# Kernel tuning notes

Measured on AMD Instinct MI355X. Metric: run time of the kernel, lower is better.

The kernel has to match this reference:

```python
import jax, jax.numpy as jnp
import numpy as np

S = 2048        # tokens (single prefill sequence)
HID = 3584      # hidden_size
H = 16          # num query heads
KV = 8          # num kv heads
D = 256         # head_dim
WINDOW = 1024   # sliding window size
CAP = 50.0      # logit softcap
SCALE = 256.0 ** -0.5   # query_pre_attn_scalar ** -0.5
THETA = 10000.0


def setup_inputs() -> dict:
    key = jax.random.key(0)
    ks = jax.random.split(key, 5)
    hidden_states = jax.random.normal(ks[0], (S, HID), dtype=jnp.float32)
    positions = jnp.arange(S, dtype=jnp.int32)
    Wq = jax.random.normal(ks[1], (HID, H * D), dtype=jnp.float32) * 0.02
    Wk = jax.random.normal(ks[2], (HID, KV * D), dtype=jnp.float32) * 0.02
    Wv = jax.random.normal(ks[3], (HID, KV * D), dtype=jnp.float32) * 0.02
    Wo = jax.random.normal(ks[4], (H * D, HID), dtype=jnp.float32) * 0.02
    return {"hidden_states": hidden_states, "positions": positions,
            "Wq": Wq, "Wk": Wk, "Wv": Wv, "Wo": Wo}


def _rope_neox(x, positions):
    # x: [S, n_heads, D]; neox-style: rotate halves, full rotary_dim == D
    half = D // 2
    inv_freq = 1.0 / (THETA ** (jnp.arange(0, half, dtype=jnp.float32) * 2.0 / D))
    freqs = positions.astype(jnp.float32)[:, None] * inv_freq[None, :]  # [S, half]
    cos = jnp.cos(freqs)[:, None, :].astype(x.dtype)
    sin = jnp.sin(freqs)[:, None, :].astype(x.dtype)
    x1, x2 = x[..., :half], x[..., half:]
    return jnp.concatenate([x1 * cos - x2 * sin, x2 * cos + x1 * sin], axis=-1)


def reference(hidden_states, positions, Wq, Wk, Wv, Wo):
    # QKV projections (no bias)
    q = (hidden_states @ Wq).reshape(S, H, D)
    k = (hidden_states @ Wk).reshape(S, KV, D)
    v = (hidden_states @ Wv).reshape(S, KV, D)
    q = _rope_neox(q, positions)
    k = _rope_neox(k, positions)
    # grouped-query attention: G query heads per kv head
    G = H // KV
    qg = q.reshape(S, KV, G, D)
    scores = jnp.einsum('qkgd,skd->kgqs', qg, k) * jnp.asarray(SCALE, q.dtype)
    # logit soft-capping
    scores = CAP * jnp.tanh(scores / CAP)
    # causal + sliding-window mask
    i = positions[:, None]
    j = positions[None, :]
    mask = (j <= i) & ((i - j) < WINDOW)   # [S, S]
    neg = jnp.finfo(scores.dtype).min
    scores = jnp.where(mask[None, None, :, :], scores, neg)
    p = jax.nn.softmax(scores, axis=-1)
    attn = jnp.einsum('kgqs,skd->qkgd', p, v).reshape(S, H * D)
    return attn @ Wo
```

## Files before the change

### kernel.cpp

```cpp
#include <hip/hip_runtime.h>
#include <stdint.h>

#define S 2048
#define HID 3584
#define NH 16
#define NKV 8
#define DH 256
#define WINDOW 1024
#define SCALE 0.0625f
#define CAP 50.0f

typedef short s16x8 __attribute__((ext_vector_type(8)));
typedef float f32x4 __attribute__((ext_vector_type(4)));

__device__ __forceinline__ short f2bf(float f) {
  union { float f; uint32_t u; } c; c.f = f;
  uint32_t u = c.u;
  uint32_t r = (u + 0x7FFFu + ((u >> 16) & 1u)) >> 16;
  return (short)r;
}
__device__ __forceinline__ float bf2f(short s) {
  union { uint32_t u; float f; } c;
  c.u = ((uint32_t)(uint16_t)s) << 16;
  return c.f;
}
__device__ __forceinline__ void gll16(const void* g, void* l) {
  __builtin_amdgcn_global_load_lds((const __attribute__((address_space(1))) void*)g,
                                   (__attribute__((address_space(3))) void*)l, 16, 0, 0);
}

__global__ void rope_table_kernel(float2* __restrict__ tbl) {
  int idx = blockIdx.x * 256 + threadIdx.x;
  int s = idx >> 7, i = idx & 127;
  float inv = __expf(-(float)i * (9.210340371976184f / 128.0f));
  float fr = (float)s * inv;
  tbl[idx] = make_float2(cosf(fr), sinf(fr));
}

__global__ void conv_hs_kernel(const float* __restrict__ src, short* __restrict__ dst) {
  int gid = blockIdx.x * 256 + threadIdx.x;
  float4 a = *(const float4*)&src[(size_t)gid * 8];
  float4 b = *(const float4*)&src[(size_t)gid * 8 + 4];
  s16x8 o;
  o[0] = f2bf(a.x); o[1] = f2bf(a.y); o[2] = f2bf(a.z); o[3] = f2bf(a.w);
  o[4] = f2bf(b.x); o[5] = f2bf(b.y); o[6] = f2bf(b.z); o[7] = f2bf(b.w);
  *(s16x8*)&dst[(size_t)gid * 8] = o;
}

__global__ __launch_bounds__(256)
void transpose_all_kernel(const float* __restrict__ Wq, const float* __restrict__ Wk,
                          const float* __restrict__ Wv, const float* __restrict__ Wo,
                          short* __restrict__ Wt, short* __restrict__ WtO)
{
  __shared__ __align__(16) short t[64][76];
  int b = blockIdx.x;
  const float* src; short* dst; int K, N, lb;
  if (b < 3584)      { src = Wq; dst = Wt;                       K = HID;  N = 4096; lb = b; }
  else if (b < 5376) { src = Wk; dst = Wt + (size_t)4096 * HID;  K = HID;  N = 2048; lb = b - 3584; }
  else if (b < 7168) { src = Wv; dst = Wt + (size_t)6144 * HID;  K = HID;  N = 2048; lb = b - 5376; }
  else               { src = Wo; dst = WtO;                      K = 4096; N = HID;  lb = b - 7168; }
  int ntn = N >> 6;
  int tn = lb % ntn, tk = lb / ntn;
  int tid = threadIdx.x;
  int c = tid & 63, rg = tid >> 6;
  #pragma unroll
  for (int i = 0; i < 4; ++i) {
    int r0 = i * 16 + rg * 4;
    short tmp[4];
    #pragma unroll
    for (int j = 0; j < 4; ++j)
      tmp[j] = f2bf(src[(size_t)(tk * 64 + r0 + j) * N + tn * 64 + c]);
    *(short4*)&t[c][r0] = *(short4*)tmp;
  }
  __syncthreads();
  #pragma unroll
  for (int it = 0; it < 2; ++it) {
    int flat = it * 256 + tid;
    int n = flat >> 3, kc = flat & 7;
    *(s16x8*)&dst[(size_t)(tn * 64 + n) * K + tk * 64 + kc * 8] = *(s16x8*)&t[n][kc * 8];
  }
}

__global__ __launch_bounds__(256)
void transpose_v_kernel(const short* __restrict__ vsb, short* __restrict__ vtb)
{
  __shared__ short t[64][74];
  int b = blockIdx.x;
  int kv = b >> 7;
  int rem = b & 127;
  int s0 = (rem >> 2) * 64, d0 = (rem & 3) * 64;
  const short* src = vsb + ((size_t)kv * S + s0) * DH + d0;
  short* dst = vtb + ((size_t)kv * DH + d0) * S + s0;
  int tid = threadIdx.x;
  int c = tid & 63, sb = (tid >> 6) * 16;
  #pragma unroll
  for (int ss = 0; ss < 16; ++ss)
    t[c][sb + ss] = src[(size_t)(sb + ss) * DH + c];
  __syncthreads();
  #pragma unroll
  for (int it = 0; it < 2; ++it) {
    int flat = it * 256 + tid;
    int r = flat >> 3, cc = (flat & 7) * 8;
    *(s16x8*)&dst[(size_t)r * S + cc] = *(s16x8*)&t[r][cc];
  }
}

__global__ __launch_bounds__(256, 2)
void qkv_gemm_kernel(const short* __restrict__ hsb, const short* __restrict__ Wt,
                     short* __restrict__ qb, short* __restrict__ kbuf,
                     short* __restrict__ vsb)
{
  __shared__ __align__(16) short Asb[256 * 64];
  __shared__ __align__(16) short Bsb[128 * 64];
  int bid = blockIdx.x;
  int i = bid >> 3;
  int bm = i & 7;
  int bn = (bid & 7) * 8 + (i >> 3);
  int m0 = bm * 256, n0 = bn * 128;
  int tid = threadIdx.x, w = tid >> 6, lane = tid & 63;
  int lr = lane & 15, lk = lane >> 4;
  int wm = (w >> 1) * 128, wn = (w & 1) * 64;
  int r7 = lr & 7;
  int abase = (wm + lr) * 64 + ((lk ^ r7) * 8);
  int bbase = (wn + lr) * 64 + ((lk ^ r7) * 8);
  int row8 = tid >> 3;
  int colsw = ((tid & 7) ^ (row8 & 7)) * 8;
  const short* srcA = hsb + (size_t)(m0 + row8) * HID + colsw;
  const short* srcB = Wt + (size_t)(n0 + row8) * HID + colsw;
  f32x4 acc[8][4] = {};
  for (int t = 0; t < HID / 64; ++t) {
    const short* sa = srcA + t * 64;
    const short* sb = srcB + t * 64;
    #pragma unroll
    for (int r = 0; r < 8; ++r)
      gll16(sa + (size_t)(r * 32) * HID, Asb + r * 2048 + w * 512);
    #pragma unroll
    for (int r = 0; r < 4; ++r)
      gll16(sb + (size_t)(r * 32) * HID, Bsb + r * 2048 + w * 512);
    __syncthreads();
    s16x8 bf[4][2];
    #pragma unroll
    for (int nf = 0; nf < 4; ++nf)
      #pragma unroll
      for (int kh = 0; kh < 2; ++kh)
        bf[nf][kh] = *(const s16x8*)&Bsb[(bbase + nf * 16 * 64) ^ (kh * 32)];
    #pragma unroll
    for (int mh = 0; mh < 2; ++mh) {
      s16x8 af[4][2];
      #pragma unroll
      for (int mf = 0; mf < 4; ++mf)
        #pragma unroll
        for (int kh = 0; kh < 2; ++kh)
          af[mf][kh] = *(const s16x8*)&Asb[(abase + (mh * 64 + mf * 16) * 64) ^ (kh * 32)];
      __builtin_amdgcn_s_setprio(1);
      #pragma unroll
      for (int mf = 0; mf < 4; ++mf)
        #pragma unroll
        for (int nf = 0; nf < 4; ++nf) {
          acc[mh * 4 + mf][nf] = __builtin_amdgcn_mfma_f32_16x16x32_bf16(
              af[mf][0], bf[nf][0], acc[mh * 4 + mf][nf], 0, 0, 0);
          acc[mh * 4 + mf][nf] = __builtin_amdgcn_mfma_f32_16x16x32_bf16(
              af[mf][1], bf[nf][1], acc[mh * 4 + mf][nf], 0, 0, 0);
        }
      __builtin_amdgcn_s_setprio(0);
    }
    __syncthreads();
  }
  int region = (n0 < 4096) ? 0 : ((n0 < 6144) ? 1 : 2);
  #pragma unroll
  for (int m = 0; m < 8; ++m) {
    int srow_b = m0 + wm + m * 16 + lk * 4;
    #pragma unroll
    for (int n = 0; n < 4; ++n) {
      int ncol = n0 + wn + n * 16 + lr;
      #pragma unroll
      for (int r = 0; r < 4; ++r) {
        int srow = srow_b + r;
        short bv = f2bf(acc[m][n][r]);
        if (region == 0) {
          int h = ncol >> 8, d = ncol & 255;
          qb[((size_t)h * S + srow) * DH + d] = bv;
        } else if (region == 1) {
          int c = ncol - 4096; int kv = c >> 8, d = c & 255;
          kbuf[((size_t)kv * S + srow) * DH + d] = bv;
        } else {
          int c = ncol - 6144; int kv = c >> 8, d = c & 255;
          vsb[((size_t)kv * S + srow) * DH + d] = bv;
        }
      }
    }
  }
}

__global__ __launch_bounds__(256)
void out_gemm_kernel(const short* __restrict__ attnb, const short* __restrict__ WtO,
                     float* __restrict__ out)
{
  __shared__ __align__(16) short Asb[128 * 64];
  __shared__ __align__(16) short Bsb[128 * 64];
  int bid = blockIdx.x;
  int flat = (bid & 7) * 56 + (bid >> 3);
  int bn = flat >> 4, bm = flat & 15;
  int m0 = bm * 128, n0 = bn * 128;
  int tid = threadIdx.x, w = tid >> 6, lane = tid & 63;
  int lr = lane & 15, lk = lane >> 4;
  int wm = (w >> 1) * 64, wn = (w & 1) * 64;
  int r7 = lr & 7;
  int abase = (wm + lr) * 64 + ((lk ^ r7) * 8);
  int bbase = (wn + lr) * 64 + ((lk ^ r7) * 8);
  int row8 = tid >> 3;
  int colsw = ((tid & 7) ^ (row8 & 7)) * 8;
  const short* srcA = attnb + (size_t)(m0 + row8) * 4096 + colsw;
  const short* srcB = WtO + (size_t)(n0 + row8) * 4096 + colsw;
  f32x4 acc[4][4] = {};
  for (int t = 0; t < 4096 / 64; ++t) {
    const short* sa = srcA + t * 64;
    const short* sb = srcB + t * 64;
    #pragma unroll
    for (int r = 0; r < 4; ++r)
      gll16(sa + (size_t)(r * 32) * 4096, Asb + r * 2048 + w * 512);
    #pragma unroll
    for (int r = 0; r < 4; ++r)
      gll16(sb + (size_t)(r * 32) * 4096, Bsb + r * 2048 + w * 512);
    __syncthreads();
    s16x8 af[4][2], bf[4][2];
    #pragma unroll
    for (int f = 0; f < 4; ++f)
      #pragma unroll
      for (int kh = 0; kh < 2; ++kh) {
        af[f][kh] = *(const s16x8*)&Asb[(abase + f * 16 * 64) ^ (kh * 32)];
        bf[f][kh] = *(const s16x8*)&Bsb[(bbase + f * 16 * 64) ^ (kh * 32)];
      }
    __builtin_amdgcn_s_setprio(1);
    #pragma unroll
    for (int mf = 0; mf < 4; ++mf)
      #pragma unroll
      for (int nf = 0; nf < 4; ++nf) {
        acc[mf][nf] = __builtin_amdgcn_mfma_f32_16x16x32_bf16(
            af[mf][0], bf[nf][0], acc[mf][nf], 0, 0, 0);
        acc[mf][nf] = __builtin_amdgcn_mfma_f32_16x16x32_bf16(
            af[mf][1], bf[nf][1], acc[mf][nf], 0, 0, 0);
      }
    __builtin_amdgcn_s_setprio(0);
    __syncthreads();
  }
  #pragma unroll
  for (int mf = 0; mf < 4; ++mf) {
    int srow_b = m0 + wm + mf * 16 + lk * 4;
    #pragma unroll
    for (int nf = 0; nf < 4; ++nf) {
      int ncol = n0 + wn + nf * 16 + lr;
      #pragma unroll
      for (int r = 0; r < 4; ++r)
        out[(size_t)(srow_b + r) * HID + ncol] = acc[mf][nf][r];
    }
  }
}

__global__ void rope_kernel(short* __restrict__ qb, short* __restrict__ kbuf,
                            const float2* __restrict__ tbl)
{
  int gid = blockIdx.x * 256 + threadIdx.x;
  int row = gid >> 4, ch = gid & 15;
  short* base = (row < NH * S) ? (qb + (size_t)row * DH)
                               : (kbuf + (size_t)(row - NH * S) * DH);
  int s = row & (S - 1);
  int i0 = ch * 8;
  s16x8 x1 = *(s16x8*)(base + i0);
  s16x8 x2 = *(s16x8*)(base + 128 + i0);
  s16x8 y1, y2;
  #pragma unroll
  for (int j = 0; j < 8; ++j) {
    float2 cs = tbl[s * 128 + i0 + j];
    float a = bf2f(x1[j]), b = bf2f(x2[j]);
    y1[j] = f2bf(a * cs.x - b * cs.y);
    y2[j] = f2bf(b * cs.x + a * cs.y);
  }
  *(s16x8*)(base + i0) = y1;
  *(s16x8*)(base + 128 + i0) = y2;
}

__global__ __launch_bounds__(512)
void attn_kernel(const short* __restrict__ qb, const short* __restrict__ kbuf,
                 const short* __restrict__ vtb, short* __restrict__ attnb)
{
  __shared__ __align__(16) short Klds[2][64][256];
  __shared__ __align__(16) short Vlds[2][256][64];
  __shared__ __align__(16) short Plds[8][16][72];
  int bid = blockIdx.x;
  int qt = 31 - (bid >> 4), h = bid & 15;
  int kv = h >> 1;
  int q0 = qt * 64;
  int tid = threadIdx.x;
  int w = tid >> 6, lane = tid & 63;
  int g = w >> 2, wsub = w & 3;
  int gtid = tid & 255;
  int lr = lane & 15, lk = lane >> 4;
  int qrow_base = q0 + wsub * 16;
  s16x8 qf[8];
  const short* qrow = qb + ((size_t)h * S + (qrow_base + lr)) * DH;
  #pragma unroll
  for (int kb = 0; kb < 8; ++kb)
    qf[kb] = *(const s16x8*)(qrow + kb * 32 + lk * 8);
  f32x4 acc_o[16] = {};
  float l_r[4] = {0.0f, 0.0f, 0.0f, 0.0f};
  int tlo = (q0 >= WINDOW - 1) ? ((q0 - (WINDOW - 1)) >> 6) : 0;
  int thi = q0 >> 6;
  const short* kbase = kbuf + (size_t)kv * S * DH;
  const short* vbase = vtb + (size_t)kv * DH * S;

  s16x8 kpf[8], vpf[8];
  auto loadRegs = [&](int t) {
    int k0 = t * 64;
    #pragma unroll
    for (int it = 0; it < 8; ++it) {
      int flat = it * 256 + gtid;
      int r = flat >> 5, cg = flat & 31;
      kpf[it] = *(const s16x8*)(kbase + (size_t)(k0 + r) * DH + cg * 8);
    }
    #pragma unroll
    for (int it = 0; it < 8; ++it) {
      int flat = it * 256 + gtid;
      int r = flat >> 3, cg = flat & 7;
      vpf[it] = *(const s16x8*)(vbase + (size_t)r * S + k0 + cg * 8);
    }
  };
  auto writeLds = [&]() {
    #pragma unroll
    for (int it = 0; it < 8; ++it) {
      int flat = it * 256 + gtid;
      int r = flat >> 5, cg = flat & 31;
      *(s16x8*)&Klds[g][r][(cg ^ (r & 7)) * 8] = kpf[it];
    }
    #pragma unroll
    for (int it = 0; it < 8; ++it) {
      int flat = it * 256 + gtid;
      int r = flat >> 3, cg = flat & 7;
      *(s16x8*)&Vlds[g][r][(cg ^ (r & 7)) * 8] = vpf[it];
    }
  };

  int tg0 = tlo + g;
  int n_all = thi - tlo + 1;
  int jmax = (n_all + 1) >> 1;
  if (tg0 <= thi) loadRegs(tg0);
  for (int j = 0; j < jmax; ++j) {
    int t = tg0 + 2 * j;
    bool active = (t <= thi);
    if (active) writeLds();
    __syncthreads();
    if (active && t + 2 <= thi) loadRegs(t + 2);
    if (active) {
      int k0 = t * 64;
      f32x4 sc4[4] = {};
      __builtin_amdgcn_s_setprio(1);
      #pragma unroll
      for (int kb = 0; kb < 8; ++kb)
        #pragma unroll
        for (int ni = 0; ni < 4; ++ni) {
          int row = ni * 16 + lr;
          s16x8 b = *(const s16x8*)&Klds[g][row][(((kb << 2) | lk) ^ (row & 7)) * 8];
          sc4[ni] = __builtin_amdgcn_mfma_f32_16x16x32_bf16(qf[kb], b, sc4[ni], 0, 0, 0);
        }
      __builtin_amdgcn_s_setprio(0);
      bool interior = (k0 + 63 <= qrow_base) && (qrow_base + 15 - k0 < WINDOW);
      #pragma unroll
      for (int ni = 0; ni < 4; ++ni)
        #pragma unroll
        for (int r = 0; r < 4; ++r) {
          float raw = sc4[ni][r];
          float e = __expf(-fabsf(raw) * (2.0f * SCALE / CAP));
          float wgt = raw > 0.0f ? e : 1.0f;
          float p = __expf(-2.0f * CAP * __fdividef(wgt, 1.0f + e));
          if (!interior) {
            int qg = qrow_base + lk * 4 + r;
            int kg = k0 + ni * 16 + lr;
            bool valid = (kg <= qg) && (qg - kg < WINDOW);
            p = valid ? p : 0.0f;
          }
          sc4[ni][r] = p;
          l_r[r] += p;
        }
      #pragma unroll
      for (int ni = 0; ni < 4; ++ni)
        #pragma unroll
        for (int r = 0; r < 4; ++r)
          Plds[w][lk * 4 + r][ni * 16 + lr] = f2bf(sc4[ni][r]);
      s16x8 pa0 = *(const s16x8*)&Plds[w][lr][lk * 8];
      s16x8 pa1 = *(const s16x8*)&Plds[w][lr][32 + lk * 8];
      __builtin_amdgcn_s_setprio(1);
      #pragma unroll
      for (int df = 0; df < 16; ++df) {
        int row = df * 16 + lr;
        s16x8 b0 = *(const s16x8*)&Vlds[g][row][((lk ^ (row & 7)) * 8)];
        s16x8 b1 = *(const s16x8*)&Vlds[g][row][(((4 + lk) ^ (row & 7)) * 8)];
        acc_o[df] = __builtin_amdgcn_mfma_f32_16x16x32_bf16(pa0, b0, acc_o[df], 0, 0, 0);
        acc_o[df] = __builtin_amdgcn_mfma_f32_16x16x32_bf16(pa1, b1, acc_o[df], 0, 0, 0);
      }
      __builtin_amdgcn_s_setprio(0);
    }
    __syncthreads();
  }
  float lsum[4];
  #pragma unroll
  for (int r = 0; r < 4; ++r) {
    float v = l_r[r];
    #pragma unroll
    for (int off = 1; off < 16; off <<= 1)
      v += __shfl_xor(v, off, 64);
    lsum[r] = v;
  }
  float* comb = (float*)&Klds[0][0][0];
  float* lcomb = (float*)&Vlds[0][0][0];
  if (g == 1) {
    #pragma unroll
    for (int df = 0; df < 16; ++df)
      #pragma unroll
      for (int r = 0; r < 4; ++r)
        comb[(size_t)(wsub * 16 + lk * 4 + r) * 256 + df * 16 + lr] = acc_o[df][r];
    if (lr == 0)
      #pragma unroll
      for (int r = 0; r < 4; ++r)
        lcomb[wsub * 16 + lk * 4 + r] = lsum[r];
  }
  __syncthreads();
  if (g == 0) {
    #pragma unroll
    for (int r = 0; r < 4; ++r) {
      int rowi = wsub * 16 + lk * 4 + r;
      float lt = lsum[r] + lcomb[rowi];
      float inv = 1.0f / lt;
      int srow = q0 + rowi;
      #pragma unroll
      for (int df = 0; df < 16; ++df) {
        float o = acc_o[df][r] + comb[(size_t)rowi * 256 + df * 16 + lr];
        attnb[(size_t)srow * (NH * DH) + h * DH + df * 16 + lr] = f2bf(o * inv);
      }
    }
  }
}

extern "C" void kernel_launch(void* const* d_in, const int* in_sizes, int n_in,
                              void* d_out, int out_size, void* d_ws, size_t ws_size,
                              hipStream_t stream) {
  const float* hs = (const float*)d_in[0];
  const float* Wq = (const float*)d_in[2];
  const float* Wk = (const float*)d_in[3];
  const float* Wv = (const float*)d_in[4];
  const float* Wo = (const float*)d_in[5];
  float* out = (float*)d_out;
  char* ws = (char*)d_ws;
  size_t off = 0;
  float2* tbl  = (float2*)(ws + off); off += 2097152;
  short* qb    = (short*)(ws + off);  off += 16777216;
  short* kbuf  = (short*)(ws + off);  off += 8388608;
  short* vtb   = (short*)(ws + off);  off += 8388608;
  short* attnb = (short*)(ws + off);  off += 16777216;
  short* hsb   = (short*)(ws + off);  off += 14680064;
  short* Wt    = (short*)(ws + off);  off += 58720256;
  short* WtO   = (short*)(ws + off);  off += 29360128;
  short* vsb   = (short*)(ws + off);  off += 8388608;

  hipLaunchKernelGGL(rope_table_kernel, dim3(1024), dim3(256), 0, stream, tbl);
  hipLaunchKernelGGL(conv_hs_kernel, dim3(3584), dim3(256), 0, stream, hs, hsb);
  hipLaunchKernelGGL(transpose_all_kernel, dim3(10752), dim3(256), 0, stream,
                     Wq, Wk, Wv, Wo, Wt, WtO);
  hipLaunchKernelGGL(qkv_gemm_kernel, dim3(512), dim3(256), 0, stream,
                     hsb, Wt, qb, kbuf, vsb);
  hipLaunchKernelGGL(transpose_v_kernel, dim3(1024), dim3(256), 0, stream,
                     vsb, vtb);
  hipLaunchKernelGGL(rope_kernel, dim3(3072), dim3(256), 0, stream, qb, kbuf, tbl);
  hipLaunchKernelGGL(attn_kernel, dim3(512), dim3(512), 0, stream,
                     qb, kbuf, vtb, attnb);
  hipLaunchKernelGGL(out_gemm_kernel, dim3(448), dim3(256), 0, stream,
                     attnb, WtO, out);
}
```

Before: 361.2 us.

## Split attention KV range across two blocks and combine partials in separate kernel

The attention kernel used to split each head's key tiles between two 256-thread groups inside one 512-thread block and merge them through LDS. It now launches twice as many 256-thread blocks, each covering alternate key tiles. Each block writes unnormalized fp32 partial outputs and row sums to workspace reused from the now-dead hidden-state and weight buffers. A new combine kernel adds the two partials, normalizes, and writes bf16. The aim is smaller blocks and less LDS per block for better occupancy and scheduling, at the cost of a large fp32 round trip through global memory and one extra launch.

```diff
diff --git a/kernel.cpp b/kernel.cpp
--- a/kernel.cpp
+++ b/kernel.cpp
@@ -280,23 +280,24 @@
   *(s16x8*)(base + 128 + i0) = y2;
 }
 
-__global__ __launch_bounds__(512)
-void attn_kernel(const short* __restrict__ qb, const short* __restrict__ kbuf,
-                 const short* __restrict__ vtb, short* __restrict__ attnb)
-{
-  __shared__ __align__(16) short Klds[2][64][256];
-  __shared__ __align__(16) short Vlds[2][256][64];
-  __shared__ __align__(16) short Plds[8][16][72];
+__global__ __launch_bounds__(256)
+void attn_partial_kernel(const short* __restrict__ qb, const short* __restrict__ kbuf,
+                         const short* __restrict__ vtb, float* __restrict__ part,
+                         float* __restrict__ partL)
+{
+  __shared__ __align__(16) short Klds[64][256];
+  __shared__ __align__(16) short Vlds[256][64];
+  __shared__ __align__(16) short Plds[4][16][72];
   int bid = blockIdx.x;
-  int qt = 31 - (bid >> 4), h = bid & 15;
+  int qt = 31 - (bid >> 5);
+  int rem = bid & 31;
+  int h = rem >> 1, half = rem & 1;
   int kv = h >> 1;
   int q0 = qt * 64;
   int tid = threadIdx.x;
   int w = tid >> 6, lane = tid & 63;
-  int g = w >> 2, wsub = w & 3;
-  int gtid = tid & 255;
   int lr = lane & 15, lk = lane >> 4;
-  int qrow_base = q0 + wsub * 16;
+  int qrow_base = q0 + w * 16;
   s16x8 qf[8];
   const short* qrow = qb + ((size_t)h * S + (qrow_base + lr)) * DH;
   #pragma unroll
@@ -314,13 +315,13 @@
     int k0 = t * 64;
     #pragma unroll
     for (int it = 0; it < 8; ++it) {
-      int flat = it * 256 + gtid;
+      int flat = it * 256 + tid;
       int r = flat >> 5, cg = flat & 31;
       kpf[it] = *(const s16x8*)(kbase + (size_t)(k0 + r) * DH + cg * 8);
     }
     #pragma unroll
     for (int it = 0; it < 8; ++it) {
-      int flat = it * 256 + gtid;
+      int flat = it * 256 + tid;
       int r = flat >> 3, cg = flat & 7;
       vpf[it] = *(const s16x8*)(vbase + (size_t)r * S + k0 + cg * 8);
     }
@@ -328,116 +329,114 @@
   auto writeLds = [&]() {
     #pragma unroll
     for (int it = 0; it < 8; ++it) {
-      int flat = it * 256 + gtid;
+      int flat = it * 256 + tid;
       int r = flat >> 5, cg = flat & 31;
-      *(s16x8*)&Klds[g][r][(cg ^ (r & 7)) * 8] = kpf[it];
+      *(s16x8*)&Klds[r][(cg ^ (r & 7)) * 8] = kpf[it];
     }
     #pragma unroll
     for (int it = 0; it < 8; ++it) {
-      int flat = it * 256 + gtid;
+      int flat = it * 256 + tid;
       int r = flat >> 3, cg = flat & 7;
-      *(s16x8*)&Vlds[g][r][(cg ^ (r & 7)) * 8] = vpf[it];
+      *(s16x8*)&Vlds[r][(cg ^ (r & 7)) * 8] = vpf[it];
     }
   };
 
-  int tg0 = tlo + g;
   int n_all = thi - tlo + 1;
-  int jmax = (n_all + 1) >> 1;
-  if (tg0 <= thi) loadRegs(tg0);
+  int tg0 = tlo + half;
+  int jmax = (n_all + 1 - half) >> 1;
+  if (jmax > 0) loadRegs(tg0);
   for (int j = 0; j < jmax; ++j) {
     int t = tg0 + 2 * j;
-    bool active = (t <= thi);
-    if (active) writeLds();
-    __syncthreads();
-    if (active && t + 2 <= thi) loadRegs(t + 2);
-    if (active) {
-      int k0 = t * 64;
-      f32x4 sc4[4] = {};
-      __builtin_amdgcn_s_setprio(1);
-      #pragma unroll
-      for (int kb = 0; kb < 8; ++kb)
-        #pragma unroll
-        for (int ni = 0; ni < 4; ++ni) {
-          int row = ni * 16 + lr;
-          s16x8 b = *(const s16x8*)&Klds[g][row][(((kb << 2) | lk) ^ (row & 7)) * 8];
-          sc4[ni] = __builtin_amdgcn_mfma_f32_16x16x32_bf16(qf[kb], b, sc4[ni], 0, 0, 0);
+    int k0 = t * 64;
+    writeLds();
+    __syncthreads();
+    if (t + 2 <= thi) loadRegs(t + 2);
+    f32x4 sc4[4] = {};
+    __builtin_amdgcn_s_setprio(1);
+    #pragma unroll
+    for (int kb = 0; kb < 8; ++kb)
+      #pragma unroll
+      for (int ni = 0; ni < 4; ++ni) {
+        int row = ni * 16 + lr;
+        s16x8 b = *(const s16x8*)&Klds[row][(((kb << 2) | lk) ^ (row & 7)) * 8];
+        sc4[ni] = __builtin_amdgcn_mfma_f32_16x16x32_bf16(qf[kb], b, sc4[ni], 0, 0, 0);
+      }
+    __builtin_amdgcn_s_setprio(0);
+    bool interior = (k0 + 63 <= qrow_base) && (qrow_base + 15 - k0 < WINDOW);
+    #pragma unroll
+    for (int ni = 0; ni < 4; ++ni)
+      #pragma unroll
+      for (int r = 0; r < 4; ++r) {
+        float raw = sc4[ni][r];
+        float e = __expf(-fabsf(raw) * (2.0f * SCALE / CAP));
+        float wgt = raw > 0.0f ? e : 1.0f;
+        float p = __expf(-2.0f * CAP * __fdividef(wgt, 1.0f + e));
+        if (!interior) {
+          int qg = qrow_base + lk * 4 + r;
+          int kg = k0 + ni * 16 + lr;
+          bool valid = (kg <= qg) && (qg - kg < WINDOW);
+          p = valid ? p : 0.0f;
         }
-      __builtin_amdgcn_s_setprio(0);
-      bool interior = (k0 + 63 <= qrow_base) && (qrow_base + 15 - k0 < WINDOW);
-      #pragma unroll
-      for (int ni = 0; ni < 4; ++ni)
-        #pragma unroll
-        for (int r = 0; r < 4; ++r) {
-          float raw = sc4[ni][r];
-          float e = __expf(-fabsf(raw) * (2.0f * SCALE / CAP));
-          float wgt = raw > 0.0f ? e : 1.0f;
-          float p = __expf(-2.0f * CAP * __fdividef(wgt, 1.0f + e));
-          if (!interior) {
-            int qg = qrow_base + lk * 4 + r;
-            int kg = k0 + ni * 16 + lr;
-            bool valid = (kg <= qg) && (qg - kg < WINDOW);
-            p = valid ? p : 0.0f;
-          }
-          sc4[ni][r] = p;
-          l_r[r] += p;
-        }
-      #pragma unroll
-      for (int ni = 0; ni < 4; ++ni)
-        #pragma unroll
-        for (int r = 0; r < 4; ++r)
-          Plds[w][lk * 4 + r][ni * 16 + lr] = f2bf(sc4[ni][r]);
-      s16x8 pa0 = *(const s16x8*)&Plds[w][lr][lk * 8];
-      s16x8 pa1 = *(const s16x8*)&Plds[w][lr][32 + lk * 8];
-      __builtin_amdgcn_s_setprio(1);
-      #pragma unroll
-      for (int df = 0; df < 16; ++df) {
-        int row = df * 16 + lr;
-        s16x8 b0 = *(const s16x8*)&Vlds[g][row][((lk ^ (row & 7)) * 8)];
-        s16x8 b1 = *(const s16x8*)&Vlds[g][row][(((4 + lk) ^ (row & 7)) * 8)];
-        acc_o[df] = __builtin_amdgcn_mfma_f32_16x16x32_bf16(pa0, b0, acc_o[df], 0, 0, 0);
-        acc_o[df] = __builtin_amdgcn_mfma_f32_16x16x32_bf16(pa1, b1, acc_o[df], 0, 0, 0);
+        sc4[ni][r] = p;
+        l_r[r] += p;
       }
-      __builtin_amdgcn_s_setprio(0);
-    }
-    __syncthreads();
-  }
-  float lsum[4];
+    #pragma unroll
+    for (int ni = 0; ni < 4; ++ni)
+      #pragma unroll
+      for (int r = 0; r < 4; ++r)
+        Plds[w][lk * 4 + r][ni * 16 + lr] = f2bf(sc4[ni][r]);
+    s16x8 pa0 = *(const s16x8*)&Plds[w][lr][lk * 8];
+    s16x8 pa1 = *(const s16x8*)&Plds[w][lr][32 + lk * 8];
+    __builtin_amdgcn_s_setprio(1);
+    #pragma unroll
+    for (int df = 0; df < 16; ++df) {
+      int row = df * 16 + lr;
+      s16x8 b0 = *(const s16x8*)&Vlds[row][((lk ^ (row & 7)) * 8)];
+      s16x8 b1 = *(const s16x8*)&Vlds[row][(((4 + lk) ^ (row & 7)) * 8)];
+      acc_o[df] = __builtin_amdgcn_mfma_f32_16x16x32_bf16(pa0, b0, acc_o[df], 0, 0, 0);
+      acc_o[df] = __builtin_amdgcn_mfma_f32_16x16x32_bf16(pa1, b1, acc_o[df], 0, 0, 0);
+    }
+    __builtin_amdgcn_s_setprio(0);
+    __syncthreads();
+  }
+  float* po = part + (size_t)half * S * 4096;
+  float* pl = partL + (size_t)half * NH * S;
   #pragma unroll
   for (int r = 0; r < 4; ++r) {
     float v = l_r[r];
     #pragma unroll
     for (int off = 1; off < 16; off <<= 1)
       v += __shfl_xor(v, off, 64);
-    lsum[r] = v;
-  }
-  float* comb = (float*)&Klds[0][0][0];
-  float* lcomb = (float*)&Vlds[0][0][0];
-  if (g == 1) {
+    int srow = qrow_base + lk * 4 + r;
+    if (lr == 0) pl[(size_t)h * S + srow] = v;
     #pragma unroll
     for (int df = 0; df < 16; ++df)
-      #pragma unroll
-      for (int r = 0; r < 4; ++r)
-        comb[(size_t)(wsub * 16 + lk * 4 + r) * 256 + df * 16 + lr] = acc_o[df][r];
-    if (lr == 0)
-      #pragma unroll
-      for (int r = 0; r < 4; ++r)
-        lcomb[wsub * 16 + lk * 4 + r] = lsum[r];
-  }
-  __syncthreads();
-  if (g == 0) {
-    #pragma unroll
-    for (int r = 0; r < 4; ++r) {
-      int rowi = wsub * 16 + lk * 4 + r;
-      float lt = lsum[r] + lcomb[rowi];
-      float inv = 1.0f / lt;
-      int srow = q0 + rowi;
-      #pragma unroll
-      for (int df = 0; df < 16; ++df) {
-        float o = acc_o[df][r] + comb[(size_t)rowi * 256 + df * 16 + lr];
-        attnb[(size_t)srow * (NH * DH) + h * DH + df * 16 + lr] = f2bf(o * inv);
-      }
-    }
-  }
+      po[(size_t)srow * 4096 + h * DH + df * 16 + lr] = acc_o[df][r];
+  }
+}
+
+__global__ __launch_bounds__(256)
+void attn_combine_kernel(const float* __restrict__ part, const float* __restrict__ partL,
+                         short* __restrict__ attnb)
+{
+  int gid = blockIdx.x * 256 + threadIdx.x;
+  size_t i0 = (size_t)gid * 8;
+  int row = (int)(i0 >> 12);
+  int col = (int)(i0 & 4095);
+  int h = col >> 8;
+  float l = partL[(size_t)h * S + row] + partL[(size_t)NH * S + (size_t)h * S + row];
+  float inv = 1.0f / l;
+  f32x4 a0 = *(const f32x4*)&part[i0];
+  f32x4 a1 = *(const f32x4*)&part[i0 + 4];
+  f32x4 b0 = *(const f32x4*)&part[(size_t)S * 4096 + i0];
+  f32x4 b1 = *(const f32x4*)&part[(size_t)S * 4096 + i0 + 4];
+  s16x8 o;
+  #pragma unroll
+  for (int j = 0; j < 4; ++j) {
+    o[j]     = f2bf((a0[j] + b0[j]) * inv);
+    o[4 + j] = f2bf((a1[j] + b1[j]) * inv);
+  }
+  *(s16x8*)&attnb[i0] = o;
 }
 
 extern "C" void kernel_launch(void* const* d_in, const int* in_sizes, int n_in,
@@ -456,10 +455,13 @@
   short* kbuf  = (short*)(ws + off);  off += 8388608;
   short* vtb   = (short*)(ws + off);  off += 8388608;
   short* attnb = (short*)(ws + off);  off += 16777216;
+  size_t off_hsb = off;
   short* hsb   = (short*)(ws + off);  off += 14680064;
   short* Wt    = (short*)(ws + off);  off += 58720256;
   short* WtO   = (short*)(ws + off);  off += 29360128;
   short* vsb   = (short*)(ws + off);  off += 8388608;
+  float* part  = (float*)(ws + off_hsb);
+  float* partL = (float*)(ws + off_hsb + (size_t)2 * S * 4096 * 4);
 
   hipLaunchKernelGGL(rope_table_kernel, dim3(1024), dim3(256), 0, stream, tbl);
   hipLaunchKernelGGL(conv_hs_kernel, dim3(3584), dim3(256), 0, stream, hs, hsb);
@@ -470,8 +472,10 @@
   hipLaunchKernelGGL(transpose_v_kernel, dim3(1024), dim3(256), 0, stream,
                      vsb, vtb);
   hipLaunchKernelGGL(rope_kernel, dim3(3072), dim3(256), 0, stream, qb, kbuf, tbl);
-  hipLaunchKernelGGL(attn_kernel, dim3(512), dim3(512), 0, stream,
-                     qb, kbuf, vtb, attnb);
+  hipLaunchKernelGGL(attn_partial_kernel, dim3(1024), dim3(256), 0, stream,
+                     qb, kbuf, vtb, part, partL);
+  hipLaunchKernelGGL(attn_combine_kernel, dim3(4096), dim3(256), 0, stream,
+                     part, partL, attnb);
   hipLaunchKernelGGL(out_gemm_kernel, dim3(448), dim3(256), 0, stream,
                      attnb, WtO, out);
 }
```

Result: slower. 379.7 us (+5.1%).
